# Kernel tuning notes

Measured on AMD Instinct MI355X. Metric: run time of the kernel, lower is better.

## Reference

```python
import jax, jax.numpy as jnp
import numpy as np

BN_EPS = 1e-5


def ball_query(pos, radius, k):
    """PointNet++-style ball query: for each point, the first k point indices
    (in index order) whose distance < radius; shorter lists are padded with the
    first valid index (self is always valid since dist=0). pos: (b,n,3).
    Returns idx: (b,n,k) int32."""
    b, n, _ = pos.shape
    sq = jnp.sum(pos * pos, axis=-1)                       # (b,n)
    d2 = sq[:, :, None] + sq[:, None, :] - 2.0 * jnp.einsum('bnc,bmc->bnm', pos, pos)
    mask = d2 < radius * radius                            # (b,n,n)
    cand = jnp.where(mask, jnp.arange(n, dtype=jnp.int32)[None, None, :], jnp.int32(n))
    # smallest-k indices in ascending order == first-k valid in index order
    neg_top, _ = jax.lax.top_k(-cand, k)                   # (b,n,k)
    idx = -neg_top
    first = idx[..., :1]
    idx = jnp.where(idx == n, first, idx)                  # pad with first neighbor
    return idx


def reference(pos, x, w1, gamma, beta, w2, b2, radius, k):
    pos = jax.lax.stop_gradient(pos)
    idx = ball_query(pos, radius, k)                       # (b,n,k)
    grouped = jax.vmap(lambda p, i: p[i])(pos, idx)        # (b,n,k,3)
    rel = grouped - pos[:, :, None, :]                     # center-subtract
    # 1x1 conv (3->3, no bias)
    h = jnp.einsum('bnkc,dc->bnkd', rel, w1)
    # BatchNorm2d (training-mode batch stats over b,k,n per channel)
    mean = jnp.mean(h, axis=(0, 1, 2))
    var = jnp.mean((h - mean) ** 2, axis=(0, 1, 2))
    h = (h - mean) * jax.lax.rsqrt(var + BN_EPS) * gamma + beta
    h = jax.nn.relu(h)
    # 1x1 conv (3->out_channel) + bias
    pe = jnp.einsum('bnkd,ed->bnke', h, w2) + b2           # (b,n,k,C)
    pe = jnp.max(pe, axis=2)                               # max over k neighbors
    return x + pe


def setup_inputs() -> dict:
    key = jax.random.key(0)
    ks = jax.random.split(key, 5)
    b, n, c, kk = 2, 8192, 64, 32
    pos = jax.random.uniform(ks[0], (b, n, 3), dtype=jnp.float32)
    x = jax.random.normal(ks[1], (b, n, c), dtype=jnp.float32)
    w1 = jax.random.normal(ks[2], (3, 3), dtype=jnp.float32) * 0.5
    gamma = jnp.ones((3,), dtype=jnp.float32)
    beta = jnp.zeros((3,), dtype=jnp.float32)
    w2 = jax.random.normal(ks[3], (c, 3), dtype=jnp.float32) * 0.5
    b2 = jnp.zeros((c,), dtype=jnp.float32)
    radius = jnp.float32(0.1)
    return {"pos": pos, "x": x, "w1": w1, "gamma": gamma, "beta": beta,
            "w2": w2, "b2": b2, "radius": radius, "k": kk}
```

## Files before the change

### kernel.cpp

```cpp
#include <hip/hip_runtime.h>
#include <math.h>

#define NPTS   8192
#define NBATCH 2
#define NQ     (NPTS * NBATCH)
#define KNB    32
#define CFEAT  64
#define BN_EPS 1e-5f

#define MAXC     1000
#define CSTR     1024
#define CAP_HIT  128

#define QBK2  16
#define NBLK2 (NQ / QBK2)

#define WS_H    0
#define WS_PART (NQ * 3 * KNB)
#define WS_CS   (WS_PART + 6 * NBLK2)
#define WS_BIN  (WS_CS + 2 * CSTR)

__device__ __forceinline__ int grid_from_r(double rd) {
    int G = (int)(1.0 / rd);
    if (G < 1) G = 1;
    while (G > 1 && 1.0 / (double)G < rd) --G;
    if (G > 10) G = 10;
    return G;
}

__device__ __forceinline__ int mbcnt64(unsigned long long m) {
    return (int)__builtin_amdgcn_mbcnt_hi((unsigned)(m >> 32),
             __builtin_amdgcn_mbcnt_lo((unsigned)m, 0u));
}

__global__ __launch_bounds__(1024) void kA_bin(
    const float* __restrict__ pos, const float* __restrict__ radius,
    float* __restrict__ ws)
{
    __shared__ int hist[MAXC];
    __shared__ int offs[MAXC + 1];
    __shared__ int cur[MAXC];
    __shared__ int scan[1024];

    const int tid = threadIdx.x;
    const int batch = blockIdx.x;
    const float* bpos = pos + (size_t)batch * NPTS * 3;
    const double rd = (double)radius[0];
    const int G = grid_from_r(rd);
    const float Gf = (float)G;
    const int NC = G * G * G;

    for (int c = tid; c < NC; c += 1024) hist[c] = 0;
    __syncthreads();
    for (int p = tid; p < NPTS; p += 1024) {
        float x = bpos[p * 3], y = bpos[p * 3 + 1], z = bpos[p * 3 + 2];
        int cx = min((int)(x * Gf), G - 1);
        int cy = min((int)(y * Gf), G - 1);
        int cz = min((int)(z * Gf), G - 1);
        atomicAdd(&hist[(cz * G + cy) * G + cx], 1);
    }
    __syncthreads();

    int v = (tid < NC) ? hist[tid] : 0;
    scan[tid] = v;
    __syncthreads();
    for (int off = 1; off < 1024; off <<= 1) {
        int t = (tid >= off) ? scan[tid - off] : 0;
        __syncthreads();
        scan[tid] += t;
        __syncthreads();
    }
    if (tid < NC) {
        int excl = (tid > 0) ? scan[tid - 1] : 0;
        offs[tid] = excl;
        cur[tid]  = excl;
    }
    if (tid == 0) offs[NC] = NPTS;
    __syncthreads();
    int* cs = (int*)ws + WS_CS + batch * CSTR;
    for (int c = tid; c <= NC; c += 1024) cs[c] = offs[c];

    float4* bin = (float4*)(ws + WS_BIN) + (size_t)batch * NPTS;
    for (int p = tid; p < NPTS; p += 1024) {
        float x = bpos[p * 3], y = bpos[p * 3 + 1], z = bpos[p * 3 + 2];
        int cx = min((int)(x * Gf), G - 1);
        int cy = min((int)(y * Gf), G - 1);
        int cz = min((int)(z * Gf), G - 1);
        int slot = atomicAdd(&cur[(cz * G + cy) * G + cx], 1);
        bin[slot] = make_float4(x, y, z, __int_as_float(p));
    }
}

__global__ __launch_bounds__(1024) void k2_query(
    const float* __restrict__ pos, const float* __restrict__ w1,
    const float* __restrict__ radius, float* __restrict__ ws)
{
    __shared__ int   hitl[QBK2][CAP_HIT];
    __shared__ int   seli[QBK2][KNB];
    __shared__ float sred[QBK2][6];

    const int tid = threadIdx.x, lane = tid & 63, wave = tid >> 6;
    const int qbase = blockIdx.x * QBK2;
    const int batch = qbase / NPTS;
    const float* bpos = pos + (size_t)batch * NPTS * 3;
    const double rd  = (double)radius[0];
    const double r2d = rd * rd;
    const int G = grid_from_r(rd);
    const float Gf = (float)G;
    const int* cs = (const int*)ws + WS_CS + batch * CSTR;
    const float4* bin = (const float4*)(ws + WS_BIN) + (size_t)batch * NPTS;

    const int qg = qbase + wave;
    const int ql = qg - batch * NPTS;
    const float qx = bpos[ql * 3], qy = bpos[ql * 3 + 1], qz = bpos[ql * 3 + 2];
    const double qxd = (double)qx, qyd = (double)qy, qzd = (double)qz;
    const double qsd = fma(qzd, qzd, fma(qyd, qyd, qxd * qxd));
    const int cx = min((int)(qx * Gf), G - 1);
    const int cy = min((int)(qy * Gf), G - 1);
    const int cz = min((int)(qz * Gf), G - 1);
    const int cx0 = max(cx - 1, 0), cx1 = min(cx + 1, G - 1);

    int hc = 0;
#pragma unroll
    for (int r = 0; r < 9; ++r) {
        const int ny = cy + (r % 3) - 1;
        const int nz = cz + (r / 3) - 1;
        if (ny < 0 || ny >= G || nz < 0 || nz >= G) continue;
        const int cb = (nz * G + ny) * G;
        const int s0 = cs[cb + cx0];
        const int s1 = cs[cb + cx1 + 1];
        for (int b0 = s0; b0 < s1; b0 += 64) {
            const int ss = b0 + lane;
            const bool act = ss < s1;
            float4 P = bin[act ? ss : s0];
            double xj = (double)P.x, yj = (double)P.y, zj = (double)P.z;
            double sqj = fma(zj, zj, fma(yj, yj, xj * xj));
            double dot = fma(zj, qzd, fma(yj, qyd, xj * qxd));
            double dd  = (qsd + sqj) - 2.0 * dot;
            bool in = act && (dd < r2d);
            unsigned long long bal = __ballot(in);
            if (in) {
                int p2 = hc + mbcnt64(bal);
                if (p2 < CAP_HIT) hitl[wave][p2] = __float_as_int(P.w);
            }
            hc += (int)__popcll(bal);
        }
    }
    if (hc > CAP_HIT) hc = CAP_HIT;

    if (hc <= KNB) {
        int v = (lane < hc) ? hitl[wave][lane] : 0x7FFFFFFF;
        int mn = v;
#pragma unroll
        for (int off = 32; off; off >>= 1) mn = min(mn, __shfl_xor(mn, off));
        if (lane < KNB) seli[wave][lane] = (lane < hc) ? v : mn;
    } else {
        int a = (lane < hc) ? hitl[wave][lane] : 0x7FFFFFFF;
        int b = (64 + lane < hc) ? hitl[wave][64 + lane] : 0x7FFFFFFF;
        int lo = 0, hi = NPTS - 1;
        while (lo < hi) {
            int mid = (lo + hi) >> 1;
            int c1 = (int)__popcll(__ballot(a <= mid)) +
                     (int)__popcll(__ballot(b <= mid));
            if (c1 >= KNB) hi = mid; else lo = mid + 1;
        }
        const int t = lo;
        unsigned long long ba = __ballot(a <= t);
        unsigned long long bb = __ballot(b <= t);
        int na = (int)__popcll(ba);
        if (a <= t) seli[wave][mbcnt64(ba)] = a;
        if (b <= t) seli[wave][na + mbcnt64(bb)] = b;
    }

    float w1r[9];
#pragma unroll
    for (int i = 0; i < 9; ++i) w1r[i] = w1[i];

    float ls0 = 0.f, ls1 = 0.f, ls2 = 0.f;
    float lq0 = 0.f, lq1 = 0.f, lq2 = 0.f;
    if (lane < KNB) {
        int j = seli[wave][lane];
        const float* pj = bpos + (size_t)j * 3;
        float rx = __fsub_rn(pj[0], qx);
        float ry = __fsub_rn(pj[1], qy);
        float rz = __fsub_rn(pj[2], qz);
        float h0 = fmaf(rz, w1r[2], fmaf(ry, w1r[1], __fmul_rn(rx, w1r[0])));
        float h1 = fmaf(rz, w1r[5], fmaf(ry, w1r[4], __fmul_rn(rx, w1r[3])));
        float h2 = fmaf(rz, w1r[8], fmaf(ry, w1r[7], __fmul_rn(rx, w1r[6])));
        float* hout = ws + WS_H + (size_t)qg * 3 * KNB;
        hout[0 * KNB + lane] = h0;
        hout[1 * KNB + lane] = h1;
        hout[2 * KNB + lane] = h2;
        ls0 = h0; ls1 = h1; ls2 = h2;
        lq0 = h0 * h0; lq1 = h1 * h1; lq2 = h2 * h2;
    }

#pragma unroll
    for (int m = 1; m < 64; m <<= 1) {
        ls0 += __shfl_xor(ls0, m); ls1 += __shfl_xor(ls1, m); ls2 += __shfl_xor(ls2, m);
        lq0 += __shfl_xor(lq0, m); lq1 += __shfl_xor(lq1, m); lq2 += __shfl_xor(lq2, m);
    }
    if (lane == 0) {
        sred[wave][0] = ls0; sred[wave][1] = ls1; sred[wave][2] = ls2;
        sred[wave][3] = lq0; sred[wave][4] = lq1; sred[wave][5] = lq2;
    }
    __syncthreads();
    if (tid < 6) {
        float s = 0.f;
#pragma unroll
        for (int w = 0; w < QBK2; ++w) s += sred[w][tid];
        ws[WS_PART + tid * NBLK2 + blockIdx.x] = s;
    }
}

__global__ __launch_bounds__(256) void k3_mlp(
    const float* __restrict__ ws, const float* __restrict__ gamma,
    const float* __restrict__ beta, const float* __restrict__ w2,
    const float* __restrict__ b2, const float* __restrict__ x,
    float* __restrict__ out)
{
    __shared__ float wred[4][6];
    __shared__ float sstat[6];
    __shared__ float g[4][KNB][3];

    const int tid = threadIdx.x, lane = tid & 63, wave = tid >> 6;

#pragma unroll
    for (int c = 0; c < 6; ++c) {
        float s = 0.f;
        for (int i = tid; i < NBLK2; i += 256) s += ws[WS_PART + c * NBLK2 + i];
#pragma unroll
        for (int m = 1; m < 64; m <<= 1) s += __shfl_xor(s, m);
        if (lane == 0) wred[wave][c] = s;
    }
    __syncthreads();
    if (tid < 3) {
        const double N = (double)((long long)NQ * KNB);
        double s = 0.0, sq = 0.0;
#pragma unroll
        for (int w = 0; w < 4; ++w) { s += wred[w][tid]; sq += wred[w][3 + tid]; }
        double mean = s / N;
        double var  = sq / N - mean * mean;
        sstat[tid]     = (float)mean;
        sstat[3 + tid] = (float)(1.0 / sqrt(var + (double)BN_EPS));
    }
    __syncthreads();

    const float m0 = sstat[0], m1 = sstat[1], m2 = sstat[2];
    const float i0 = sstat[3], i1 = sstat[4], i2 = sstat[5];
    const float g0c = gamma[0], g1c = gamma[1], g2c = gamma[2];
    const float b0c = beta[0],  b1c = beta[1],  b2c = beta[2];
    const float w20 = w2[lane * 3 + 0];
    const float w21 = w2[lane * 3 + 1];
    const float w22 = w2[lane * 3 + 2];
    const float bias = b2[lane];

    const int qg0 = blockIdx.x * QBK2 + wave * 4;
#pragma unroll
    for (int q = 0; q < 4; ++q) {
        const int qg = qg0 + q;
        if (lane < KNB) {
            const float* hin = ws + WS_H + (size_t)qg * 3 * KNB;
            float h0 = hin[0 * KNB + lane];
            float h1 = hin[1 * KNB + lane];
            float h2 = hin[2 * KNB + lane];
            float n0 = __fadd_rn(__fmul_rn(__fmul_rn(__fsub_rn(h0, m0), i0), g0c), b0c);
            float n1 = __fadd_rn(__fmul_rn(__fmul_rn(__fsub_rn(h1, m1), i1), g1c), b1c);
            float n2 = __fadd_rn(__fmul_rn(__fmul_rn(__fsub_rn(h2, m2), i2), g2c), b2c);
            g[wave][lane][0] = fmaxf(n0, 0.0f);
            g[wave][lane][1] = fmaxf(n1, 0.0f);
            g[wave][lane][2] = fmaxf(n2, 0.0f);
        }
        __syncthreads();
        float m = -INFINITY;
#pragma unroll 4
        for (int kk = 0; kk < KNB; ++kk) {
            float ga = g[wave][kk][0], gb = g[wave][kk][1], gc = g[wave][kk][2];
            float pe = __fadd_rn(fmaf(gc, w22, fmaf(gb, w21, __fmul_rn(ga, w20))), bias);
            m = fmaxf(m, pe);
        }
        const size_t o = (size_t)qg * CFEAT + lane;
        out[o] = __fadd_rn(x[o], m);
        __syncthreads();
    }
}

extern "C" void kernel_launch(void* const* d_in, const int* in_sizes, int n_in,
                              void* d_out, int out_size, void* d_ws, size_t ws_size,
                              hipStream_t stream) {
    (void)in_sizes; (void)n_in; (void)out_size; (void)ws_size;
    const float* pos    = (const float*)d_in[0];
    const float* x      = (const float*)d_in[1];
    const float* w1     = (const float*)d_in[2];
    const float* gamma  = (const float*)d_in[3];
    const float* beta   = (const float*)d_in[4];
    const float* w2     = (const float*)d_in[5];
    const float* b2     = (const float*)d_in[6];
    const float* radius = (const float*)d_in[7];
    float* out = (float*)d_out;
    float* ws  = (float*)d_ws;

    hipLaunchKernelGGL(kA_bin,   dim3(NBATCH), dim3(1024), 0, stream, pos, radius, ws);
    hipLaunchKernelGGL(k2_query, dim3(NBLK2),  dim3(1024), 0, stream, pos, w1, radius, ws);
    hipLaunchKernelGGL(k3_mlp,   dim3(NBLK2),  dim3(256),  0, stream,
                       ws, gamma, beta, w2, b2, x, out);
}
```

Before: 63.40 us.

## Process ball query per grid cell with shared-memory neighbor candidate staging

The query kernel now launches one block per grid cell instead of one wave per query. Each block stages the 3x3x3 neighborhood's binned points into LDS once, then its four waves loop over the queries in that cell, reading candidates from LDS instead of global memory. Hit indices are packed with their LDS slot so selected neighbors can be fetched from LDS rather than from pos. The costs are load imbalance across cells, idle blocks for empty or out-of-range cells, and a CAPC cap of 896 on candidates that could truncate dense neighborhoods.

Result: slower. 72.10 us (+13.7%).

```diff
diff --git a/kernel.cpp b/kernel.cpp
--- a/kernel.cpp
+++ b/kernel.cpp
@@ -11,13 +11,16 @@
 #define MAXC     1000
 #define CSTR     1024
 #define CAP_HIT  128
-
-#define QBK2  16
-#define NBLK2 (NQ / QBK2)
+#define CAPC     896
+
+#define NPBLK (NBATCH * MAXC)
+
+#define QBK3  16
+#define NBLK3 (NQ / QBK3)
 
 #define WS_H    0
 #define WS_PART (NQ * 3 * KNB)
-#define WS_CS   (WS_PART + 6 * NBLK2)
+#define WS_CS   (WS_PART + 6 * NPBLK)
 #define WS_BIN  (WS_CS + 2 * CSTR)
 
 __device__ __forceinline__ int grid_from_r(double rd) {
@@ -91,48 +94,84 @@
     }
 }
 
-__global__ __launch_bounds__(1024) void k2_query(
-    const float* __restrict__ pos, const float* __restrict__ w1,
-    const float* __restrict__ radius, float* __restrict__ ws)
+__global__ __launch_bounds__(256) void k2_cell(
+    const float* __restrict__ w1, const float* __restrict__ radius,
+    float* __restrict__ ws)
 {
-    __shared__ int   hitl[QBK2][CAP_HIT];
-    __shared__ int   seli[QBK2][KNB];
-    __shared__ float sred[QBK2][6];
+    __shared__ float4 sc[CAPC];
+    __shared__ int    hitl[4][CAP_HIT];
+    __shared__ int    seli[4][KNB];
+    __shared__ float  sred[4][6];
 
     const int tid = threadIdx.x, lane = tid & 63, wave = tid >> 6;
-    const int qbase = blockIdx.x * QBK2;
-    const int batch = qbase / NPTS;
-    const float* bpos = pos + (size_t)batch * NPTS * 3;
+    const int batch = blockIdx.x / MAXC;
+    const int cell  = blockIdx.x % MAXC;
     const double rd  = (double)radius[0];
     const double r2d = rd * rd;
     const int G = grid_from_r(rd);
-    const float Gf = (float)G;
+    const int NC = G * G * G;
+
+    if (cell >= NC) {
+        if (tid < 6) ws[WS_PART + tid * NPBLK + blockIdx.x] = 0.f;
+        return;
+    }
     const int* cs = (const int*)ws + WS_CS + batch * CSTR;
     const float4* bin = (const float4*)(ws + WS_BIN) + (size_t)batch * NPTS;
 
-    const int qg = qbase + wave;
-    const int ql = qg - batch * NPTS;
-    const float qx = bpos[ql * 3], qy = bpos[ql * 3 + 1], qz = bpos[ql * 3 + 2];
-    const double qxd = (double)qx, qyd = (double)qy, qzd = (double)qz;
-    const double qsd = fma(qzd, qzd, fma(qyd, qyd, qxd * qxd));
-    const int cx = min((int)(qx * Gf), G - 1);
-    const int cy = min((int)(qy * Gf), G - 1);
-    const int cz = min((int)(qz * Gf), G - 1);
+    const int cx = cell % G, cy = (cell / G) % G, cz = cell / (G * G);
+    const int q0 = cs[cell], q1 = cs[cell + 1];
+    const int nq = q1 - q0;
+    if (nq == 0) {
+        if (tid < 6) ws[WS_PART + tid * NPBLK + blockIdx.x] = 0.f;
+        return;
+    }
     const int cx0 = max(cx - 1, 0), cx1 = min(cx + 1, G - 1);
 
-    int hc = 0;
+    int rs0[9], rlen[9], rpref[9];
+    int tot = 0, qoff = 0;
 #pragma unroll
     for (int r = 0; r < 9; ++r) {
-        const int ny = cy + (r % 3) - 1;
-        const int nz = cz + (r / 3) - 1;
-        if (ny < 0 || ny >= G || nz < 0 || nz >= G) continue;
-        const int cb = (nz * G + ny) * G;
-        const int s0 = cs[cb + cx0];
-        const int s1 = cs[cb + cx1 + 1];
-        for (int b0 = s0; b0 < s1; b0 += 64) {
+        int ny = cy + r % 3 - 1, nz = cz + r / 3 - 1;
+        int s0 = 0, len = 0;
+        if (ny >= 0 && ny < G && nz >= 0 && nz < G) {
+            int cb = (nz * G + ny) * G;
+            s0  = cs[cb + cx0];
+            len = cs[cb + cx1 + 1] - s0;
+        }
+        rs0[r] = s0; rlen[r] = len; rpref[r] = tot;
+        if (r == 4) qoff = tot + (q0 - s0);
+        tot += len;
+    }
+    if (tot > CAPC) tot = CAPC;
+
+#pragma unroll
+    for (int r = 0; r < 9; ++r) {
+        const int len = rlen[r], p0 = rpref[r], s0 = rs0[r];
+        for (int i = tid; i < len; i += 256) {
+            int d = p0 + i;
+            if (d < CAPC) sc[d] = bin[s0 + i];
+        }
+    }
+    __syncthreads();
+
+    float w1r[9];
+#pragma unroll
+    for (int i = 0; i < 9; ++i) w1r[i] = w1[i];
+
+    float ls0 = 0.f, ls1 = 0.f, ls2 = 0.f;
+    float lq0 = 0.f, lq1 = 0.f, lq2 = 0.f;
+
+    for (int qi = wave; qi < nq; qi += 4) {
+        const float4 Q = sc[qoff + qi];
+        const int qidx = __float_as_int(Q.w);
+        const double qxd = (double)Q.x, qyd = (double)Q.y, qzd = (double)Q.z;
+        const double qsd = fma(qzd, qzd, fma(qyd, qyd, qxd * qxd));
+
+        int hc = 0;
+        for (int b0 = 0; b0 < tot; b0 += 64) {
             const int ss = b0 + lane;
-            const bool act = ss < s1;
-            float4 P = bin[act ? ss : s0];
+            const bool act = ss < tot;
+            float4 P = sc[act ? ss : 0];
             double xj = (double)P.x, yj = (double)P.y, zj = (double)P.z;
             double sqj = fma(zj, zj, fma(yj, yj, xj * xj));
             double dot = fma(zj, qzd, fma(yj, qyd, xj * qxd));
@@ -141,58 +180,53 @@
             unsigned long long bal = __ballot(in);
             if (in) {
                 int p2 = hc + mbcnt64(bal);
-                if (p2 < CAP_HIT) hitl[wave][p2] = __float_as_int(P.w);
+                if (p2 < CAP_HIT)
+                    hitl[wave][p2] = (__float_as_int(P.w) << 10) | ss;
             }
             hc += (int)__popcll(bal);
         }
-    }
-    if (hc > CAP_HIT) hc = CAP_HIT;
-
-    if (hc <= KNB) {
-        int v = (lane < hc) ? hitl[wave][lane] : 0x7FFFFFFF;
-        int mn = v;
-#pragma unroll
-        for (int off = 32; off; off >>= 1) mn = min(mn, __shfl_xor(mn, off));
-        if (lane < KNB) seli[wave][lane] = (lane < hc) ? v : mn;
-    } else {
-        int a = (lane < hc) ? hitl[wave][lane] : 0x7FFFFFFF;
-        int b = (64 + lane < hc) ? hitl[wave][64 + lane] : 0x7FFFFFFF;
-        int lo = 0, hi = NPTS - 1;
-        while (lo < hi) {
-            int mid = (lo + hi) >> 1;
-            int c1 = (int)__popcll(__ballot(a <= mid)) +
-                     (int)__popcll(__ballot(b <= mid));
-            if (c1 >= KNB) hi = mid; else lo = mid + 1;
-        }
-        const int t = lo;
-        unsigned long long ba = __ballot(a <= t);
-        unsigned long long bb = __ballot(b <= t);
-        int na = (int)__popcll(ba);
-        if (a <= t) seli[wave][mbcnt64(ba)] = a;
-        if (b <= t) seli[wave][na + mbcnt64(bb)] = b;
-    }
-
-    float w1r[9];
-#pragma unroll
-    for (int i = 0; i < 9; ++i) w1r[i] = w1[i];
-
-    float ls0 = 0.f, ls1 = 0.f, ls2 = 0.f;
-    float lq0 = 0.f, lq1 = 0.f, lq2 = 0.f;
-    if (lane < KNB) {
-        int j = seli[wave][lane];
-        const float* pj = bpos + (size_t)j * 3;
-        float rx = __fsub_rn(pj[0], qx);
-        float ry = __fsub_rn(pj[1], qy);
-        float rz = __fsub_rn(pj[2], qz);
-        float h0 = fmaf(rz, w1r[2], fmaf(ry, w1r[1], __fmul_rn(rx, w1r[0])));
-        float h1 = fmaf(rz, w1r[5], fmaf(ry, w1r[4], __fmul_rn(rx, w1r[3])));
-        float h2 = fmaf(rz, w1r[8], fmaf(ry, w1r[7], __fmul_rn(rx, w1r[6])));
-        float* hout = ws + WS_H + (size_t)qg * 3 * KNB;
-        hout[0 * KNB + lane] = h0;
-        hout[1 * KNB + lane] = h1;
-        hout[2 * KNB + lane] = h2;
-        ls0 = h0; ls1 = h1; ls2 = h2;
-        lq0 = h0 * h0; lq1 = h1 * h1; lq2 = h2 * h2;
+        if (hc > CAP_HIT) hc = CAP_HIT;
+
+        if (hc <= KNB) {
+            int v = (lane < hc) ? hitl[wave][lane] : 0x7FFFFFFF;
+            int mn = v;
+#pragma unroll
+            for (int off = 32; off; off >>= 1) mn = min(mn, __shfl_xor(mn, off));
+            if (lane < KNB) seli[wave][lane] = (lane < hc) ? v : mn;
+        } else {
+            int a = (lane < hc) ? hitl[wave][lane] : 0x7FFFFFFF;
+            int b = (64 + lane < hc) ? hitl[wave][64 + lane] : 0x7FFFFFFF;
+            int lo = 0, hi = (NPTS << 10) - 1;
+            while (lo < hi) {
+                int mid = (lo + hi) >> 1;
+                int c1 = (int)__popcll(__ballot(a <= mid)) +
+                         (int)__popcll(__ballot(b <= mid));
+                if (c1 >= KNB) hi = mid; else lo = mid + 1;
+            }
+            const int t = lo;
+            unsigned long long ba = __ballot(a <= t);
+            unsigned long long bb = __ballot(b <= t);
+            int na = (int)__popcll(ba);
+            if (a <= t) seli[wave][mbcnt64(ba)] = a;
+            if (b <= t) seli[wave][na + mbcnt64(bb)] = b;
+        }
+
+        if (lane < KNB) {
+            int packed = seli[wave][lane];
+            float4 PJ = sc[packed & 1023];
+            float rx = __fsub_rn(PJ.x, Q.x);
+            float ry = __fsub_rn(PJ.y, Q.y);
+            float rz = __fsub_rn(PJ.z, Q.z);
+            float h0 = fmaf(rz, w1r[2], fmaf(ry, w1r[1], __fmul_rn(rx, w1r[0])));
+            float h1 = fmaf(rz, w1r[5], fmaf(ry, w1r[4], __fmul_rn(rx, w1r[3])));
+            float h2 = fmaf(rz, w1r[8], fmaf(ry, w1r[7], __fmul_rn(rx, w1r[6])));
+            float* hout = ws + WS_H + (size_t)(batch * NPTS + qidx) * 3 * KNB;
+            hout[0 * KNB + lane] = h0;
+            hout[1 * KNB + lane] = h1;
+            hout[2 * KNB + lane] = h2;
+            ls0 += h0; ls1 += h1; ls2 += h2;
+            lq0 += h0 * h0; lq1 += h1 * h1; lq2 += h2 * h2;
+        }
     }
 
 #pragma unroll
@@ -206,10 +240,8 @@
     }
     __syncthreads();
     if (tid < 6) {
-        float s = 0.f;
-#pragma unroll
-        for (int w = 0; w < QBK2; ++w) s += sred[w][tid];
-        ws[WS_PART + tid * NBLK2 + blockIdx.x] = s;
+        float s = sred[0][tid] + sred[1][tid] + sred[2][tid] + sred[3][tid];
+        ws[WS_PART + tid * NPBLK + blockIdx.x] = s;
     }
 }
 
@@ -228,7 +260,7 @@
 #pragma unroll
     for (int c = 0; c < 6; ++c) {
         float s = 0.f;
-        for (int i = tid; i < NBLK2; i += 256) s += ws[WS_PART + c * NBLK2 + i];
+        for (int i = tid; i < NPBLK; i += 256) s += ws[WS_PART + c * NPBLK + i];
 #pragma unroll
         for (int m = 1; m < 64; m <<= 1) s += __shfl_xor(s, m);
         if (lane == 0) wred[wave][c] = s;
@@ -255,7 +287,7 @@
     const float w22 = w2[lane * 3 + 2];
     const float bias = b2[lane];
 
-    const int qg0 = blockIdx.x * QBK2 + wave * 4;
+    const int qg0 = blockIdx.x * QBK3 + wave * 4;
 #pragma unroll
     for (int q = 0; q < 4; ++q) {
         const int qg = qg0 + q;
@@ -301,7 +333,7 @@
     float* ws  = (float*)d_ws;
 
     hipLaunchKernelGGL(kA_bin,   dim3(NBATCH), dim3(1024), 0, stream, pos, radius, ws);
-    hipLaunchKernelGGL(k2_query, dim3(NBLK2),  dim3(1024), 0, stream, pos, w1, radius, ws);
-    hipLaunchKernelGGL(k3_mlp,   dim3(NBLK2),  dim3(256),  0, stream,
+    hipLaunchKernelGGL(k2_cell,  dim3(NPBLK),  dim3(256),  0, stream, w1, radius, ws);
+    hipLaunchKernelGGL(k3_mlp,   dim3(NBLK3),  dim3(256),  0, stream,
                        ws, gamma, beta, w2, b2, x, out);
 }
```

## Shrink query blocks to 4 waves and use wave-shuffle scan in binning

Applied to the files above, without the earlier changes.

The query kernel now runs 256-thread blocks with 4 queries each instead of 16, which gives four times as many blocks for better CU occupancy and load balance. The MLP kernel keeps its 16-query blocks through a separate block constant. The binning kernel drops to 256 threads and replaces the 1024-wide shared-memory Hillis-Steele scan (many barriers) with a per-thread 4-cell sum, a wave shuffle scan and a cross-wave combine. The BN partial-sum buffer now holds four times as many entries, which the MLP kernel must reduce over, and the binning kernel has fewer threads for its point loops.

Result: slower. 86.31 us (+36.1%).

```diff
diff --git a/kernel.cpp b/kernel.cpp
--- a/kernel.cpp
+++ b/kernel.cpp
@@ -12,8 +12,11 @@
 #define CSTR     1024
 #define CAP_HIT  128
 
-#define QBK2  16
+#define QBK2  4
 #define NBLK2 (NQ / QBK2)
+
+#define QBK3  16
+#define NBLK3 (NQ / QBK3)
 
 #define WS_H    0
 #define WS_PART (NQ * 3 * KNB)
@@ -33,16 +36,16 @@
              __builtin_amdgcn_mbcnt_lo((unsigned)m, 0u));
 }
 
-__global__ __launch_bounds__(1024) void kA_bin(
+__global__ __launch_bounds__(256) void kA_bin(
     const float* __restrict__ pos, const float* __restrict__ radius,
     float* __restrict__ ws)
 {
     __shared__ int hist[MAXC];
-    __shared__ int offs[MAXC + 1];
+    __shared__ int offs[MAXC];
     __shared__ int cur[MAXC];
-    __shared__ int scan[1024];
-
-    const int tid = threadIdx.x;
+    __shared__ int wtot[4];
+
+    const int tid = threadIdx.x, lane = tid & 63, wave = tid >> 6;
     const int batch = blockIdx.x;
     const float* bpos = pos + (size_t)batch * NPTS * 3;
     const double rd = (double)radius[0];
@@ -50,9 +53,9 @@
     const float Gf = (float)G;
     const int NC = G * G * G;
 
-    for (int c = tid; c < NC; c += 1024) hist[c] = 0;
-    __syncthreads();
-    for (int p = tid; p < NPTS; p += 1024) {
+    for (int c = tid; c < NC; c += 256) hist[c] = 0;
+    __syncthreads();
+    for (int p = tid; p < NPTS; p += 256) {
         float x = bpos[p * 3], y = bpos[p * 3 + 1], z = bpos[p * 3 + 2];
         int cx = min((int)(x * Gf), G - 1);
         int cy = min((int)(y * Gf), G - 1);
@@ -61,27 +64,35 @@
     }
     __syncthreads();
 
-    int v = (tid < NC) ? hist[tid] : 0;
-    scan[tid] = v;
-    __syncthreads();
-    for (int off = 1; off < 1024; off <<= 1) {
-        int t = (tid >= off) ? scan[tid - off] : 0;
-        __syncthreads();
-        scan[tid] += t;
-        __syncthreads();
-    }
-    if (tid < NC) {
-        int excl = (tid > 0) ? scan[tid - 1] : 0;
-        offs[tid] = excl;
-        cur[tid]  = excl;
-    }
-    if (tid == 0) offs[NC] = NPTS;
-    __syncthreads();
+    const int c0 = tid * 4;
+    int h0 = (c0 + 0 < NC) ? hist[c0 + 0] : 0;
+    int h1 = (c0 + 1 < NC) ? hist[c0 + 1] : 0;
+    int h2 = (c0 + 2 < NC) ? hist[c0 + 2] : 0;
+    int h3 = (c0 + 3 < NC) ? hist[c0 + 3] : 0;
+    const int tsum = h0 + h1 + h2 + h3;
+    int incl = tsum;
+#pragma unroll
+    for (int off = 1; off < 64; off <<= 1) {
+        int v = __shfl_up(incl, off);
+        if (lane >= off) incl += v;
+    }
+    if (lane == 63) wtot[wave] = incl;
+    __syncthreads();
+    int wbase = 0;
+#pragma unroll
+    for (int w = 0; w < 4; ++w) wbase += (w < wave) ? wtot[w] : 0;
+    int base = wbase + incl - tsum;
+    if (c0 + 0 < NC) { offs[c0 + 0] = base; cur[c0 + 0] = base; base += h0; }
+    if (c0 + 1 < NC) { offs[c0 + 1] = base; cur[c0 + 1] = base; base += h1; }
+    if (c0 + 2 < NC) { offs[c0 + 2] = base; cur[c0 + 2] = base; base += h2; }
+    if (c0 + 3 < NC) { offs[c0 + 3] = base; cur[c0 + 3] = base; base += h3; }
+    __syncthreads();
+
     int* cs = (int*)ws + WS_CS + batch * CSTR;
-    for (int c = tid; c <= NC; c += 1024) cs[c] = offs[c];
+    for (int c = tid; c <= NC; c += 256) cs[c] = (c < NC) ? offs[c] : NPTS;
 
     float4* bin = (float4*)(ws + WS_BIN) + (size_t)batch * NPTS;
-    for (int p = tid; p < NPTS; p += 1024) {
+    for (int p = tid; p < NPTS; p += 256) {
         float x = bpos[p * 3], y = bpos[p * 3 + 1], z = bpos[p * 3 + 2];
         int cx = min((int)(x * Gf), G - 1);
         int cy = min((int)(y * Gf), G - 1);
@@ -91,7 +102,7 @@
     }
 }
 
-__global__ __launch_bounds__(1024) void k2_query(
+__global__ __launch_bounds__(256) void k2_query(
     const float* __restrict__ pos, const float* __restrict__ w1,
     const float* __restrict__ radius, float* __restrict__ ws)
 {
@@ -206,9 +217,7 @@
     }
     __syncthreads();
     if (tid < 6) {
-        float s = 0.f;
-#pragma unroll
-        for (int w = 0; w < QBK2; ++w) s += sred[w][tid];
+        float s = sred[0][tid] + sred[1][tid] + sred[2][tid] + sred[3][tid];
         ws[WS_PART + tid * NBLK2 + blockIdx.x] = s;
     }
 }
@@ -255,7 +264,7 @@
     const float w22 = w2[lane * 3 + 2];
     const float bias = b2[lane];
 
-    const int qg0 = blockIdx.x * QBK2 + wave * 4;
+    const int qg0 = blockIdx.x * QBK3 + wave * 4;
 #pragma unroll
     for (int q = 0; q < 4; ++q) {
         const int qg = qg0 + q;
@@ -300,8 +309,8 @@
     float* out = (float*)d_out;
     float* ws  = (float*)d_ws;
 
-    hipLaunchKernelGGL(kA_bin,   dim3(NBATCH), dim3(1024), 0, stream, pos, radius, ws);
-    hipLaunchKernelGGL(k2_query, dim3(NBLK2),  dim3(1024), 0, stream, pos, w1, radius, ws);
-    hipLaunchKernelGGL(k3_mlp,   dim3(NBLK2),  dim3(256),  0, stream,
+    hipLaunchKernelGGL(kA_bin,   dim3(NBATCH), dim3(256), 0, stream, pos, radius, ws);
+    hipLaunchKernelGGL(k2_query, dim3(NBLK2),  dim3(256), 0, stream, pos, w1, radius, ws);
+    hipLaunchKernelGGL(k3_mlp,   dim3(NBLK3),  dim3(256), 0, stream,
                        ws, gamma, beta, w2, b2, x, out);
 }
```
